# Optimization experiments

Hardware: AMD Instinct MI355X
Metric: run time of the kernel (lower is better)

## Reference

```python
import jax, jax.numpy as jnp
import numpy as np

B, T, C, H = 512, 40, 512, 512


def _gru_dir(x, Wih, Whh, bih, bhh):
    """Single-direction PyTorch-convention GRU. x: [B,T,C] -> [B,T,H]."""
    Hh = Whh.shape[1]
    # precompute input projections for all timesteps: [B,T,3H]
    gx = jnp.einsum('btc,gc->btg', x, Wih) + bih

    def step(h, gxt):
        gh = h @ Whh.T + bhh  # [B,3H]
        r = jax.nn.sigmoid(gxt[:, :Hh] + gh[:, :Hh])
        z = jax.nn.sigmoid(gxt[:, Hh:2 * Hh] + gh[:, Hh:2 * Hh])
        n = jnp.tanh(gxt[:, 2 * Hh:] + r * gh[:, 2 * Hh:])
        h_new = (1.0 - z) * n + z * h
        return h_new, h_new

    h0 = jnp.zeros((x.shape[0], Hh), x.dtype)
    _, ys = jax.lax.scan(step, h0, jnp.swapaxes(gx, 0, 1))  # [T,B,H]
    return jnp.swapaxes(ys, 0, 1)


def setup_inputs() -> dict:
    key = jax.random.key(0)
    ks = jax.random.split(key, 10)
    s = 1.0 / np.sqrt(H)  # PyTorch default init scale
    lengths = jax.random.randint(ks[0], (B,), 5, T + 1)
    valid = jnp.arange(T)[None, :] < lengths[:, None]  # [B,T]
    ref_expr = jax.random.normal(ks[1], (B, T, C), jnp.float32) * valid[..., None]
    mk = lambda k, shape: jax.random.uniform(k, shape, jnp.float32, -s, s)
    return {
        'ref_expr': ref_expr,
        'Wih_f': mk(ks[2], (3 * H, C)), 'Whh_f': mk(ks[3], (3 * H, H)),
        'bih_f': mk(ks[4], (3 * H,)), 'bhh_f': mk(ks[5], (3 * H,)),
        'Wih_b': mk(ks[6], (3 * H, C)), 'Whh_b': mk(ks[7], (3 * H, H)),
        'bih_b': mk(ks[8], (3 * H,)), 'bhh_b': mk(ks[9], (3 * H,)),
    }


def reference(ref_expr, Wih_f, Whh_f, bih_f, bhh_f, Wih_b, Whh_b, bih_b, bhh_b):
    # padded positions are all-zero embedding vectors -> masked out
    valid = jnp.any(ref_expr != 0, axis=-1)  # [B,T], True = keep
    y_fwd = _gru_dir(ref_expr, Wih_f, Whh_f, bih_f, bhh_f)
    y_bwd = _gru_dir(ref_expr[:, ::-1], Wih_b, Whh_b, bih_b, bhh_b)[:, ::-1]
    y_word = jnp.concatenate([y_fwd, y_bwd], axis=-1)  # [B,T,2H]
    # masked max pooling over valid tokens (output_type='max')
    neg = jnp.finfo(y_word.dtype).min
    y = jnp.max(jnp.where(valid[..., None], y_word, neg), axis=1, keepdims=True)
    return y  # [B,1,2H]
```

## Files before the change

### kernel.cpp

```cpp
#include <hip/hip_runtime.h>
#include <hip/hip_bf16.h>
#include <float.h>

#define BB 512
#define TT 40
#define CC 512
#define HH 512

typedef short bf16x8 __attribute__((ext_vector_type(8)));
typedef float f32x4 __attribute__((ext_vector_type(4)));
typedef unsigned short ushortx8 __attribute__((ext_vector_type(8)));

#define LDSH 49152
#define LDSF 98304
#define LDSTOT 98320

__device__ __forceinline__ unsigned short f2bf(float f){
  union { float f; unsigned int i; } v; v.f = f;
  unsigned int r = v.i + 0x7fffu + ((v.i >> 16) & 1u);
  return (unsigned short)(r >> 16);
}

__device__ __forceinline__ bf16x8 load_sc0(const unsigned short* p){
  bf16x8 r;
  asm volatile("global_load_dwordx4 %0, %1, off sc0" : "=v"(r) : "v"(p));
  return r;
}
#define WAITV(N) do { asm volatile("s_waitcnt vmcnt(" #N ")" ::: "memory"); \
                      __builtin_amdgcn_sched_barrier(0); } while(0)

__device__ __forceinline__ float fast_sigmoid(float x){
  return __builtin_amdgcn_rcpf(1.f + __expf(-x));
}
__device__ __forceinline__ float fast_tanh(float x){
  return 1.f - 2.f*__builtin_amdgcn_rcpf(__expf(2.f*x) + 1.f);
}

__global__ void prep_x_kernel(const float* __restrict__ x, unsigned short* __restrict__ xb,
                              float* __restrict__ maskT){
  int w = blockIdx.x*4 + (threadIdx.x>>6);
  int lane = threadIdx.x & 63;
  const float* src = x + (size_t)w*CC + lane*8;
  f32x4 a = *(const f32x4*)(src);
  f32x4 b = *(const f32x4*)(src+4);
  ushortx8 o;
  o[0]=f2bf(a[0]); o[1]=f2bf(a[1]); o[2]=f2bf(a[2]); o[3]=f2bf(a[3]);
  o[4]=f2bf(b[0]); o[5]=f2bf(b[1]); o[6]=f2bf(b[2]); o[7]=f2bf(b[3]);
  *(ushortx8*)(xb + (size_t)w*CC + lane*8) = o;
  bool nz = (a[0]!=0.f)||(a[1]!=0.f)||(a[2]!=0.f)||(a[3]!=0.f)||
            (b[0]!=0.f)||(b[1]!=0.f)||(b[2]!=0.f)||(b[3]!=0.f);
  unsigned long long bal = __ballot(nz);
  if (lane==0){
    int b_ = w / TT, t_ = w % TT;
    maskT[t_*BB + b_] = bal ? 1.0f : 0.0f;
  }
}

__global__ void cvt_kernel(const float* __restrict__ src, unsigned short* __restrict__ dst, int n8){
  int i = blockIdx.x*blockDim.x + threadIdx.x;
  if (i < n8){
    f32x4 a = *(const f32x4*)(src + i*8);
    f32x4 b = *(const f32x4*)(src + i*8 + 4);
    ushortx8 o;
    o[0]=f2bf(a[0]); o[1]=f2bf(a[1]); o[2]=f2bf(a[2]); o[3]=f2bf(a[3]);
    o[4]=f2bf(b[0]); o[5]=f2bf(b[1]); o[6]=f2bf(b[2]); o[7]=f2bf(b[3]);
    *(ushortx8*)(dst + i*8) = o;
  }
}

__global__ void init_h_kernel(unsigned short* __restrict__ hb, unsigned int* __restrict__ ctr){
  int i = blockIdx.x*blockDim.x + threadIdx.x;
  hb[i] = 0;
  if (i < 8) ctr[i*32] = 0u;
}

__global__ __launch_bounds__(256) void gru_persist_kernel(
    const unsigned short* __restrict__ xb,
    const unsigned short* __restrict__ wihF, const unsigned short* __restrict__ whhF,
    const unsigned short* __restrict__ wihB, const unsigned short* __restrict__ whhB,
    const float* __restrict__ bihF, const float* __restrict__ bhhF,
    const float* __restrict__ bihB, const float* __restrict__ bhhB,
    const float* __restrict__ maskT,
    unsigned short* __restrict__ hb,
    float* __restrict__ out, unsigned int* __restrict__ ctr)
{
  const int bid   = blockIdx.x;
  const int grp   = bid & 7;
  const int strip = bid >> 3;
  const int dir   = grp >> 2;
  const int bslab = grp & 3;
  const int b0 = bslab * 128;
  const int n0 = strip * 16;
  unsigned int* myctr = ctr + grp*32;

  const unsigned short* wih = dir ? wihB : wihF;
  const unsigned short* whh = dir ? whhB : whhF;
  const float* bih = dir ? bihB : bihF;
  const float* bhh = dir ? bhhB : bhhF;

  const int tid  = threadIdx.x;
  const int lane = tid & 63;
  const int lr   = lane & 15;
  const int lkg  = lane >> 4;
  const int wv   = tid >> 6;
  const int wrow = wv * 32;

  __shared__ __align__(16) char smem[LDSTOT];
  unsigned int* arrive = (unsigned int*)(smem + LDSF);
  unsigned int* goflag = (unsigned int*)(smem + LDSF + 8);

  for (int q = tid; q < 6144; q += 256) {
    const int p_  = q >= 3072;
    const int r_  = p_ ? (q - 3072) : q;
    const int row = r_ >> 6;
    const int kc  = (r_ & 63) * 8;
    const unsigned short* src =
        (p_ ? whh : wih) + ((size_t)((row>>4)*HH + n0 + (row&15)))*512 + kc;
    *(ushortx8*)(smem + p_*LDSH + row*1024 + ((kc*2) ^ ((row&15)<<4))) =
        *(const ushortx8*)src;
  }
  if (tid == 0){ arrive[0] = 0u; goflag[0] = 0u; }
  __syncthreads();

  const int jj = n0 + lr;
  const float br  = bih[jj]        + bhh[jj];
  const float bz  = bih[HH + jj]   + bhh[HH + jj];
  const float bnx = bih[2*HH + jj];
  const float bnh = bhh[2*HH + jj];

  float omax[2][4], hreg[2][4];
  #pragma unroll
  for (int mf=0; mf<2; ++mf)
    #pragma unroll
    for (int j=0; j<4; ++j){ omax[mf][j] = -FLT_MAX; hreg[mf][j] = 0.f; }

  const int swz = lr << 4;
  const char* wbx = smem + lr*1024;
  const char* wbh = smem + LDSH + lr*1024;

  for (int t = 0; t < TT; ++t) {
    const int tx = dir ? (TT-1-t) : t;
    const int bi = t & 1;
    const unsigned short* hbin = hb + (size_t)(dir*2 + bi)      * (BB*HH);
    unsigned short* hbout      = hb + (size_t)(dir*2 + (bi^1))  * (BB*HH);

    f32x4 ar[2], az[2], anx[2], anh[2];
    #pragma unroll
    for (int mf=0; mf<2; ++mf){ ar[mf]=0.f; az[mf]=0.f; anx[mf]=0.f; anh[mf]=0.f; }

    const unsigned short* xr0 = xb + ((size_t)(b0 + wrow + lr     )*TT + tx)*CC;
    const unsigned short* xr1 = xb + ((size_t)(b0 + wrow + 16 + lr)*TT + tx)*CC;

    #pragma unroll
    for (int kk = 0; kk < 16; ++kk) {
      const int ko = kk*32 + lkg*8;
      bf16x8 a0 = *(const bf16x8*)(xr0 + ko);
      bf16x8 a1 = *(const bf16x8*)(xr1 + ko);
      const int kbx = (ko*2) ^ swz;
      bf16x8 brf = *(const bf16x8*)(wbx +         kbx);
      bf16x8 bzf = *(const bf16x8*)(wbx + 16384 + kbx);
      bf16x8 bnf = *(const bf16x8*)(wbx + 32768 + kbx);
      ar[0]  = __builtin_amdgcn_mfma_f32_16x16x32_bf16(a0, brf, ar[0],0,0,0);
      ar[1]  = __builtin_amdgcn_mfma_f32_16x16x32_bf16(a1, brf, ar[1],0,0,0);
      az[0]  = __builtin_amdgcn_mfma_f32_16x16x32_bf16(a0, bzf, az[0],0,0,0);
      az[1]  = __builtin_amdgcn_mfma_f32_16x16x32_bf16(a1, bzf, az[1],0,0,0);
      anx[0] = __builtin_amdgcn_mfma_f32_16x16x32_bf16(a0, bnf, anx[0],0,0,0);
      anx[1] = __builtin_amdgcn_mfma_f32_16x16x32_bf16(a1, bnf, anx[1],0,0,0);
    }

    const float* mrow = maskT + tx*BB + b0 + wrow + lkg*4;
    const f32x4 mk0 = *(const f32x4*)(mrow);
    const f32x4 mk1 = *(const f32x4*)(mrow + 16);

    if (t > 0) {
      if (wv == 0 && lane == 0) {
        const unsigned int tgt = 32u*(unsigned)t;
        unsigned int spin = 0;
        while (__hip_atomic_load(myctr, __ATOMIC_RELAXED, __HIP_MEMORY_SCOPE_AGENT) < tgt
               && ++spin < (1u<<24))
          __builtin_amdgcn_s_sleep(2);
        __hip_atomic_store(goflag, (unsigned)t, __ATOMIC_RELEASE, __HIP_MEMORY_SCOPE_WORKGROUP);
      }
      unsigned int spin = 0;
      while (__hip_atomic_load(goflag, __ATOMIC_ACQUIRE, __HIP_MEMORY_SCOPE_WORKGROUP) < (unsigned)t
             && ++spin < (1u<<24))
        __builtin_amdgcn_s_sleep(1);
    }

    WAITV(0);

    const unsigned short* hr0 = hbin + (size_t)(b0 + wrow + lr     )*HH;
    const unsigned short* hr1 = hbin + (size_t)(b0 + wrow + 16 + lr)*HH;
    bf16x8 ph[4][2];
    #pragma unroll
    for (int q = 0; q < 4; ++q){
      ph[q][0] = load_sc0(hr0 + q*32 + lkg*8);
      ph[q][1] = load_sc0(hr1 + q*32 + lkg*8);
    }
    #pragma unroll
    for (int kk = 0; kk < 16; ++kk) {
      const int ko = kk*32 + lkg*8;
      const int kbx = (ko*2) ^ swz;
      bf16x8 brf = *(const bf16x8*)(wbh +         kbx);
      bf16x8 bzf = *(const bf16x8*)(wbh + 16384 + kbx);
      bf16x8 bnf = *(const bf16x8*)(wbh + 32768 + kbx);
      if (kk < 13)      { WAITV(6); }
      else if (kk == 13){ WAITV(4); }
      else if (kk == 14){ WAITV(2); }
      else              { WAITV(0); }
      bf16x8 c0 = ph[kk&3][0];
      bf16x8 c1 = ph[kk&3][1];
      ar[0]  = __builtin_amdgcn_mfma_f32_16x16x32_bf16(c0, brf, ar[0],0,0,0);
      ar[1]  = __builtin_amdgcn_mfma_f32_16x16x32_bf16(c1, brf, ar[1],0,0,0);
      az[0]  = __builtin_amdgcn_mfma_f32_16x16x32_bf16(c0, bzf, az[0],0,0,0);
      az[1]  = __builtin_amdgcn_mfma_f32_16x16x32_bf16(c1, bzf, az[1],0,0,0);
      anh[0] = __builtin_amdgcn_mfma_f32_16x16x32_bf16(c0, bnf, anh[0],0,0,0);
      anh[1] = __builtin_amdgcn_mfma_f32_16x16x32_bf16(c1, bnf, anh[1],0,0,0);
      if (kk < 12) {
        ph[kk&3][0] = load_sc0(hr0 + (kk+4)*32 + lkg*8);
        ph[kk&3][1] = load_sc0(hr1 + (kk+4)*32 + lkg*8);
      }
    }

    #pragma unroll
    for (int mf=0; mf<2; ++mf){
      const f32x4 mk = mf ? mk1 : mk0;
      #pragma unroll
      for (int j=0; j<4; ++j){
        const int b = b0 + wrow + mf*16 + lkg*4 + j;
        const float rg = fast_sigmoid(ar[mf][j] + br);
        const float zg = fast_sigmoid(az[mf][j] + bz);
        const float ng = fast_tanh(anx[mf][j] + bnx + rg*(anh[mf][j] + bnh));
        const float hn = (1.f - zg)*ng + zg*hreg[mf][j];
        hreg[mf][j] = hn;
        hbout[(size_t)b*HH + jj] = f2bf(hn);
        const float cand = (mk[j] != 0.f) ? hn : -FLT_MAX;
        omax[mf][j] = fmaxf(omax[mf][j], cand);
      }
    }

    if (t < TT-1) {
      WAITV(0);
      if (lane == 0)
        __hip_atomic_fetch_add(arrive, 1u, __ATOMIC_RELEASE, __HIP_MEMORY_SCOPE_WORKGROUP);
      if (wv == 0 && lane == 0) {
        const unsigned int tgt = 4u*(unsigned)(t+1);
        unsigned int spin = 0;
        while (__hip_atomic_load(arrive, __ATOMIC_ACQUIRE, __HIP_MEMORY_SCOPE_WORKGROUP) < tgt
               && ++spin < (1u<<24))
          __builtin_amdgcn_s_sleep(1);
        __hip_atomic_fetch_add(myctr, 1u, __ATOMIC_RELAXED, __HIP_MEMORY_SCOPE_AGENT);
      }
    }
  }

  #pragma unroll
  for (int mf=0; mf<2; ++mf)
    #pragma unroll
    for (int j=0; j<4; ++j){
      const int b = b0 + wrow + mf*16 + lkg*4 + j;
      out[(size_t)b*(2*HH) + dir*HH + jj] = omax[mf][j];
    }
}

extern "C" void kernel_launch(void* const* d_in, const int* in_sizes, int n_in,
                              void* d_out, int out_size, void* d_ws, size_t ws_size,
                              hipStream_t stream) {
  const float* x    = (const float*)d_in[0];
  const float* WihF = (const float*)d_in[1];
  const float* WhhF = (const float*)d_in[2];
  const float* bihF = (const float*)d_in[3];
  const float* bhhF = (const float*)d_in[4];
  const float* WihB = (const float*)d_in[5];
  const float* WhhB = (const float*)d_in[6];
  const float* bihB = (const float*)d_in[7];
  const float* bhhB = (const float*)d_in[8];
  float* out = (float*)d_out;

  char* ws = (char*)d_ws;
  unsigned short* xb    = (unsigned short*)(ws);
  unsigned short* wb    = (unsigned short*)(ws + 20971520);
  unsigned short* wihFb = wb;
  unsigned short* whhFb = wb + 786432;
  unsigned short* wihBb = wb + 2*786432;
  unsigned short* whhBb = wb + 3*786432;
  float* maskT = (float*)(ws + 27262976);
  unsigned short* hb = (unsigned short*)(ws + 27344896);
  unsigned int* ctr  = (unsigned int*)(ws + 29442048);

  prep_x_kernel<<<BB*TT/4, 256, 0, stream>>>(x, xb, maskT);
  cvt_kernel<<<384, 256, 0, stream>>>(WihF, wihFb, 98304);
  cvt_kernel<<<384, 256, 0, stream>>>(WhhF, whhFb, 98304);
  cvt_kernel<<<384, 256, 0, stream>>>(WihB, wihBb, 98304);
  cvt_kernel<<<384, 256, 0, stream>>>(WhhB, whhBb, 98304);
  init_h_kernel<<<4096, 256, 0, stream>>>(hb, ctr);

  gru_persist_kernel<<<256, 256, 0, stream>>>(xb, wihFb, whhFb, wihBb, whhBb,
                                              bihF, bhhF, bihB, bhhB,
                                              maskT, hb, out, ctr);
}
```

Baseline: 370.9 us.

## Double waves per block, one 16-row M tile per wave, direct global spin

The persistent GRU block grows from 4 to 8 waves. Each wave now covers 16 batch rows instead of 32, so per-wave MFMA chains and register use are halved and more waves are available to hide latency. The single-leader goflag handoff is removed: every thread now polls the global step counter itself, and the arrival target is raised to 8. This may add contention on the global atomic, and launch_bounds(512,2) tightens the register budget.

After: 335.8 us (median of 2 runs). 9.5% less time.

```diff
diff --git a/kernel.cpp b/kernel.cpp
--- a/kernel.cpp
+++ b/kernel.cpp
@@ -74,7 +74,7 @@
   if (i < 8) ctr[i*32] = 0u;
 }
 
-__global__ __launch_bounds__(256) void gru_persist_kernel(
+__global__ __launch_bounds__(512, 2) void gru_persist_kernel(
     const unsigned short* __restrict__ xb,
     const unsigned short* __restrict__ wihF, const unsigned short* __restrict__ whhF,
     const unsigned short* __restrict__ wihB, const unsigned short* __restrict__ whhB,
@@ -103,13 +103,12 @@
   const int lr   = lane & 15;
   const int lkg  = lane >> 4;
   const int wv   = tid >> 6;
-  const int wrow = wv * 32;
+  const int wrow = wv * 16;
 
   __shared__ __align__(16) char smem[LDSTOT];
   unsigned int* arrive = (unsigned int*)(smem + LDSF);
-  unsigned int* goflag = (unsigned int*)(smem + LDSF + 8);
-
-  for (int q = tid; q < 6144; q += 256) {
+
+  for (int q = tid; q < 6144; q += 512) {
     const int p_  = q >= 3072;
     const int r_  = p_ ? (q - 3072) : q;
     const int row = r_ >> 6;
@@ -119,7 +118,7 @@
     *(ushortx8*)(smem + p_*LDSH + row*1024 + ((kc*2) ^ ((row&15)<<4))) =
         *(const ushortx8*)src;
   }
-  if (tid == 0){ arrive[0] = 0u; goflag[0] = 0u; }
+  if (tid == 0) arrive[0] = 0u;
   __syncthreads();
 
   const int jj = n0 + lr;
@@ -128,11 +127,9 @@
   const float bnx = bih[2*HH + jj];
   const float bnh = bhh[2*HH + jj];
 
-  float omax[2][4], hreg[2][4];
+  float omax[4], hreg[4];
   #pragma unroll
-  for (int mf=0; mf<2; ++mf)
-    #pragma unroll
-    for (int j=0; j<4; ++j){ omax[mf][j] = -FLT_MAX; hreg[mf][j] = 0.f; }
+  for (int j=0; j<4; ++j){ omax[j] = -FLT_MAX; hreg[j] = 0.f; }
 
   const int swz = lr << 4;
   const char* wbx = smem + lr*1024;
@@ -144,59 +141,40 @@
     const unsigned short* hbin = hb + (size_t)(dir*2 + bi)      * (BB*HH);
     unsigned short* hbout      = hb + (size_t)(dir*2 + (bi^1))  * (BB*HH);
 
-    f32x4 ar[2], az[2], anx[2], anh[2];
-    #pragma unroll
-    for (int mf=0; mf<2; ++mf){ ar[mf]=0.f; az[mf]=0.f; anx[mf]=0.f; anh[mf]=0.f; }
-
-    const unsigned short* xr0 = xb + ((size_t)(b0 + wrow + lr     )*TT + tx)*CC;
-    const unsigned short* xr1 = xb + ((size_t)(b0 + wrow + 16 + lr)*TT + tx)*CC;
+    f32x4 ar = 0.f, az = 0.f, anx = 0.f, anh = 0.f;
+
+    const unsigned short* xr0 = xb + ((size_t)(b0 + wrow + lr)*TT + tx)*CC;
 
     #pragma unroll
     for (int kk = 0; kk < 16; ++kk) {
       const int ko = kk*32 + lkg*8;
       bf16x8 a0 = *(const bf16x8*)(xr0 + ko);
-      bf16x8 a1 = *(const bf16x8*)(xr1 + ko);
       const int kbx = (ko*2) ^ swz;
       bf16x8 brf = *(const bf16x8*)(wbx +         kbx);
       bf16x8 bzf = *(const bf16x8*)(wbx + 16384 + kbx);
       bf16x8 bnf = *(const bf16x8*)(wbx + 32768 + kbx);
-      ar[0]  = __builtin_amdgcn_mfma_f32_16x16x32_bf16(a0, brf, ar[0],0,0,0);
-      ar[1]  = __builtin_amdgcn_mfma_f32_16x16x32_bf16(a1, brf, ar[1],0,0,0);
-      az[0]  = __builtin_amdgcn_mfma_f32_16x16x32_bf16(a0, bzf, az[0],0,0,0);
-      az[1]  = __builtin_amdgcn_mfma_f32_16x16x32_bf16(a1, bzf, az[1],0,0,0);
-      anx[0] = __builtin_amdgcn_mfma_f32_16x16x32_bf16(a0, bnf, anx[0],0,0,0);
-      anx[1] = __builtin_amdgcn_mfma_f32_16x16x32_bf16(a1, bnf, anx[1],0,0,0);
-    }
-
-    const float* mrow = maskT + tx*BB + b0 + wrow + lkg*4;
-    const f32x4 mk0 = *(const f32x4*)(mrow);
-    const f32x4 mk1 = *(const f32x4*)(mrow + 16);
+      ar  = __builtin_amdgcn_mfma_f32_16x16x32_bf16(a0, brf, ar,0,0,0);
+      az  = __builtin_amdgcn_mfma_f32_16x16x32_bf16(a0, bzf, az,0,0,0);
+      anx = __builtin_amdgcn_mfma_f32_16x16x32_bf16(a0, bnf, anx,0,0,0);
+    }
+
+    const f32x4 mk = *(const f32x4*)(maskT + tx*BB + b0 + wrow + lkg*4);
 
     if (t > 0) {
-      if (wv == 0 && lane == 0) {
-        const unsigned int tgt = 32u*(unsigned)t;
-        unsigned int spin = 0;
-        while (__hip_atomic_load(myctr, __ATOMIC_RELAXED, __HIP_MEMORY_SCOPE_AGENT) < tgt
-               && ++spin < (1u<<24))
-          __builtin_amdgcn_s_sleep(2);
-        __hip_atomic_store(goflag, (unsigned)t, __ATOMIC_RELEASE, __HIP_MEMORY_SCOPE_WORKGROUP);
-      }
+      const unsigned int tgt = 32u*(unsigned)t;
       unsigned int spin = 0;
-      while (__hip_atomic_load(goflag, __ATOMIC_ACQUIRE, __HIP_MEMORY_SCOPE_WORKGROUP) < (unsigned)t
+      while (__hip_atomic_load(myctr, __ATOMIC_RELAXED, __HIP_MEMORY_SCOPE_AGENT) < tgt
              && ++spin < (1u<<24))
         __builtin_amdgcn_s_sleep(1);
     }
 
     WAITV(0);
 
-    const unsigned short* hr0 = hbin + (size_t)(b0 + wrow + lr     )*HH;
-    const unsigned short* hr1 = hbin + (size_t)(b0 + wrow + 16 + lr)*HH;
-    bf16x8 ph[4][2];
-    #pragma unroll
-    for (int q = 0; q < 4; ++q){
-      ph[q][0] = load_sc0(hr0 + q*32 + lkg*8);
-      ph[q][1] = load_sc0(hr1 + q*32 + lkg*8);
-    }
+    const unsigned short* hr0 = hbin + (size_t)(b0 + wrow + lr)*HH;
+    bf16x8 ph[4];
+    #pragma unroll
+    for (int q = 0; q < 4; ++q)
+      ph[q] = load_sc0(hr0 + q*32 + lkg*8);
     #pragma unroll
     for (int kk = 0; kk < 16; ++kk) {
       const int ko = kk*32 + lkg*8;
@@ -204,39 +182,29 @@
       bf16x8 brf = *(const bf16x8*)(wbh +         kbx);
       bf16x8 bzf = *(const bf16x8*)(wbh + 16384 + kbx);
       bf16x8 bnf = *(const bf16x8*)(wbh + 32768 + kbx);
-      if (kk < 13)      { WAITV(6); }
-      else if (kk == 13){ WAITV(4); }
-      else if (kk == 14){ WAITV(2); }
+      if (kk < 13)      { WAITV(3); }
+      else if (kk == 13){ WAITV(2); }
+      else if (kk == 14){ WAITV(1); }
       else              { WAITV(0); }
-      bf16x8 c0 = ph[kk&3][0];
-      bf16x8 c1 = ph[kk&3][1];
-      ar[0]  = __builtin_amdgcn_mfma_f32_16x16x32_bf16(c0, brf, ar[0],0,0,0);
-      ar[1]  = __builtin_amdgcn_mfma_f32_16x16x32_bf16(c1, brf, ar[1],0,0,0);
-      az[0]  = __builtin_amdgcn_mfma_f32_16x16x32_bf16(c0, bzf, az[0],0,0,0);
-      az[1]  = __builtin_amdgcn_mfma_f32_16x16x32_bf16(c1, bzf, az[1],0,0,0);
-      anh[0] = __builtin_amdgcn_mfma_f32_16x16x32_bf16(c0, bnf, anh[0],0,0,0);
-      anh[1] = __builtin_amdgcn_mfma_f32_16x16x32_bf16(c1, bnf, anh[1],0,0,0);
-      if (kk < 12) {
-        ph[kk&3][0] = load_sc0(hr0 + (kk+4)*32 + lkg*8);
-        ph[kk&3][1] = load_sc0(hr1 + (kk+4)*32 + lkg*8);
-      }
-    }
-
-    #pragma unroll
-    for (int mf=0; mf<2; ++mf){
-      const f32x4 mk = mf ? mk1 : mk0;
-      #pragma unroll
-      for (int j=0; j<4; ++j){
-        const int b = b0 + wrow + mf*16 + lkg*4 + j;
-        const float rg = fast_sigmoid(ar[mf][j] + br);
-        const float zg = fast_sigmoid(az[mf][j] + bz);
-        const float ng = fast_tanh(anx[mf][j] + bnx + rg*(anh[mf][j] + bnh));
-        const float hn = (1.f - zg)*ng + zg*hreg[mf][j];
-        hreg[mf][j] = hn;
-        hbout[(size_t)b*HH + jj] = f2bf(hn);
-        const float cand = (mk[j] != 0.f) ? hn : -FLT_MAX;
-        omax[mf][j] = fmaxf(omax[mf][j], cand);
-      }
+      bf16x8 c0 = ph[kk&3];
+      ar  = __builtin_amdgcn_mfma_f32_16x16x32_bf16(c0, brf, ar,0,0,0);
+      az  = __builtin_amdgcn_mfma_f32_16x16x32_bf16(c0, bzf, az,0,0,0);
+      anh = __builtin_amdgcn_mfma_f32_16x16x32_bf16(c0, bnf, anh,0,0,0);
+      if (kk < 12)
+        ph[kk&3] = load_sc0(hr0 + (kk+4)*32 + lkg*8);
+    }
+
+    #pragma unroll
+    for (int j=0; j<4; ++j){
+      const int b = b0 + wrow + lkg*4 + j;
+      const float rg = fast_sigmoid(ar[j] + br);
+      const float zg = fast_sigmoid(az[j] + bz);
+      const float ng = fast_tanh(anx[j] + bnx + rg*(anh[j] + bnh));
+      const float hn = (1.f - zg)*ng + zg*hreg[j];
+      hreg[j] = hn;
+      hbout[(size_t)b*HH + jj] = f2bf(hn);
+      const float cand = (mk[j] != 0.f) ? hn : -FLT_MAX;
+      omax[j] = fmaxf(omax[j], cand);
     }
 
     if (t < TT-1) {
@@ -244,7 +212,7 @@
       if (lane == 0)
         __hip_atomic_fetch_add(arrive, 1u, __ATOMIC_RELEASE, __HIP_MEMORY_SCOPE_WORKGROUP);
       if (wv == 0 && lane == 0) {
-        const unsigned int tgt = 4u*(unsigned)(t+1);
+        const unsigned int tgt = 8u*(unsigned)(t+1);
         unsigned int spin = 0;
         while (__hip_atomic_load(arrive, __ATOMIC_ACQUIRE, __HIP_MEMORY_SCOPE_WORKGROUP) < tgt
                && ++spin < (1u<<24))
@@ -255,12 +223,10 @@
   }
 
   #pragma unroll
-  for (int mf=0; mf<2; ++mf)
-    #pragma unroll
-    for (int j=0; j<4; ++j){
-      const int b = b0 + wrow + mf*16 + lkg*4 + j;
-      out[(size_t)b*(2*HH) + dir*HH + jj] = omax[mf][j];
-    }
+  for (int j=0; j<4; ++j){
+    const int b = b0 + wrow + lkg*4 + j;
+    out[(size_t)b*(2*HH) + dir*HH + jj] = omax[j];
+  }
 }
 
 extern "C" void kernel_launch(void* const* d_in, const int* in_sizes, int n_in,
@@ -295,7 +261,7 @@
   cvt_kernel<<<384, 256, 0, stream>>>(WhhB, whhBb, 98304);
   init_h_kernel<<<4096, 256, 0, stream>>>(hb, ctr);
 
-  gru_persist_kernel<<<256, 256, 0, stream>>>(xb, wihFb, whhFb, wihBb, whhBb,
+  gru_persist_kernel<<<256, 512, 0, stream>>>(xb, wihFb, whhFb, wihBb, whhBb,
                                               bihF, bhhF, bihB, bhhB,
                                               maskT, hb, out, ctr);
 }
```
